# Kernel optimization log

Measured on AMD Instinct MI355X. Metric: run time of the kernel, lower is better.

## Reference

```python
import jax, jax.numpy as jnp
import numpy as np


def setup_inputs() -> dict:
    key = jax.random.key(0)
    ks = jax.random.split(key, 8)
    B, N, D = 8, 2048, 128
    s = 1.0 / float(np.sqrt(D))
    node = jax.random.normal(ks[0], (B, N, D), dtype=jnp.float32)
    node_mask = jax.random.randint(ks[1], (B, N), 0, 2, dtype=jnp.int32)
    punctuation_graph = jax.random.randint(ks[2], (B, N, N), 0, 2, dtype=jnp.int32)
    w_nw = jax.random.uniform(ks[3], (1, D), jnp.float32, -s, s)
    b_nw = jax.random.uniform(ks[4], (1,), jnp.float32, -s, s)
    w_self = jax.random.uniform(ks[5], (D, D), jnp.float32, -s, s)
    b_self = jax.random.uniform(ks[6], (D,), jnp.float32, -s, s)
    w_punct = jax.random.uniform(ks[7], (D, D), jnp.float32, -s, s)
    return {"node": node, "node_mask": node_mask, "punctuation_graph": punctuation_graph,
            "w_nw": w_nw, "b_nw": b_nw, "w_self": w_self, "b_self": b_self,
            "w_punct": w_punct, "iteration_steps": 2}


def reference(node, node_mask, punctuation_graph, w_nw, b_nw, w_self, b_self, w_punct, iteration_steps):
    B, N, D = node.shape
    # dd_graph = mask outer product with zeroed diagonal; graph = dd_graph * punctuation_graph
    eye = jnp.eye(N, dtype=punctuation_graph.dtype)
    dd = node_mask[:, None, :] * node_mask[:, :, None] * (1 - eye)[None, :, :]  # [B,N,N]
    graph = dd * punctuation_graph  # [B,N,N] int, binary
    nbr_num = graph.sum(-1)  # [B,N]
    # replace_masked_values(nbr_num, nbr_num>=1, 1): nodes with no neighbors get denom 1
    nbr_f = jnp.where(nbr_num >= 1, nbr_num.astype(node.dtype), jnp.asarray(1.0, node.dtype))
    gmask = graph > 0
    weights = []
    x = node
    for _ in range(iteration_steps):  # small fixed step count
        dw = jax.nn.sigmoid(jnp.einsum('bnd,od->bno', x, w_nw) + b_nw)[..., 0]  # [B,N]
        weights.append(dw)
        self_info = jnp.einsum('bnd,ed->bne', x, w_self) + b_self  # [B,N,D]
        info_p = jnp.einsum('bnd,ed->bne', x, w_punct)  # [B,N,D]
        # node_weight[b,i,j] = dw[b,j] where graph[b,i,j] else 0
        nw = jnp.where(gmask, dw[:, None, :], jnp.asarray(0.0, x.dtype))  # [B,N,N]
        agg = jnp.einsum('bnm,bmd->bnd', nw, info_p) / nbr_f[..., None]
        x = jax.nn.relu(self_info + agg)
    all_weight = jnp.stack(weights, axis=1)  # [B, steps, N]
    return x, all_weight
```

## Files before the change

### kernel.cpp

```cpp
#include <hip/hip_runtime.h>
#include <hip/hip_bf16.h>

#define BB 8
#define NN 2048
#define DD 128

typedef __attribute__((ext_vector_type(8))) __bf16 bf16x8;
typedef __attribute__((ext_vector_type(4))) float f32x4;
typedef __attribute__((ext_vector_type(4))) int   i32x4;

static __device__ __forceinline__ unsigned short f2bf(float f) {
    union { float f; unsigned u; } v; v.f = f;
    unsigned r = (v.u + 0x7FFFu + ((v.u >> 16) & 1u)) >> 16;
    return (unsigned short)r;
}
static __device__ __forceinline__ float bf2f(unsigned short b) {
    union { unsigned u; float f; } v; v.u = ((unsigned)b) << 16;
    return v.f;
}

__global__ __launch_bounds__(256) void kernP(
    const int* __restrict__ punct, const int* __restrict__ mask,
    unsigned* __restrict__ pk, float* __restrict__ scale_g, float* __restrict__ pdm_g)
{
    const int t = threadIdx.x;
    const int wave = t >> 6, lane = t & 63;
    const int row_g = blockIdx.x * 4 + wave;
    const int b = row_g >> 11;
    const int i = row_g & (NN - 1);

    const int* prow = punct + (size_t)row_g * NN;
    const int* mrow = mask + (size_t)b * NN;

    unsigned pk0 = 0, pk1 = 0;
    int acc = 0;
    #pragma unroll 4
    for (int w = 0; w < 32; ++w) {
        const int col = w * 64 + lane;
        const int p = prow[col];
        const int m = mrow[col];
        const int pred = (p & m) & 1;
        unsigned long long bal = __ballot(pred);
        if (lane == w) { pk0 = (unsigned)bal; pk1 = (unsigned)(bal >> 32); }
        acc += pred + ((col == i ? pred : 0) << 16);
    }
    #pragma unroll
    for (int o = 32; o > 0; o >>= 1) acc += __shfl_xor(acc, o, 64);

    if (lane < 32) {
        uint2 w2; w2.x = pk0; w2.y = pk1;
        *(uint2*)(pk + (size_t)row_g * 64 + 2 * lane) = w2;
    }

    if (lane == 0) {
        const int nall = acc & 0xFFFF;
        const int pdm  = acc >> 16;
        const int mi   = mrow[i];
        const int nbr  = nall - pdm;
        scale_g[row_g] = mi ? 1.f / (float)(nbr < 1 ? 1 : nbr) : 0.f;
        pdm_g[row_g]   = (float)pdm;
    }
}

__global__ __launch_bounds__(256) void kernB(
    const float* __restrict__ x,
    const float* __restrict__ w_nw,  const float* __restrict__ b_nw,
    const float* __restrict__ w_self,const float* __restrict__ b_self,
    const float* __restrict__ w_punct,
    float* __restrict__ si_out,
    unsigned short* __restrict__ yne_out,
    unsigned short* __restrict__ yT_out,
    float* __restrict__ aw_out)
{
    __shared__ unsigned short xt[64*32];
    __shared__ unsigned short wst[128*32];
    __shared__ unsigned short wpt[128*32];
    __shared__ float wnw_l[DD];
    __shared__ float red[256];
    __shared__ float dw_l[64];
    __shared__ unsigned short ytl[128*72];

    const int t  = threadIdx.x;
    const int n0 = blockIdx.x * 64;
    const int b  = n0 >> 11;
    const int nb = n0 & (NN - 1);

    if (t < DD) wnw_l[t] = w_nw[t];
    __syncthreads();

    const int wave = t >> 6, lane = t & 63;
    const int wm = wave >> 1, wn = wave & 1;
    const int quad = lane >> 4, l16 = lane & 15;

    const int n_loc = t >> 2, dq = t & 3;
    const int we = t >> 1,   wh = t & 1;

    f32x4 accs[2][4] = {}; f32x4 accp[2][4] = {};
    float dwpart = 0.f;

    #pragma unroll
    for (int kk = 0; kk < 4; ++kk) {
        const int k0 = kk * 32;
        {
            const float* xs = x + (size_t)(n0 + n_loc) * DD + k0 + dq * 8;
            f32x4 a = *(const f32x4*)xs;
            f32x4 c = *(const f32x4*)(xs + 4);
            const float* wv = &wnw_l[k0 + dq * 8];
            dwpart += a.x*wv[0] + a.y*wv[1] + a.z*wv[2] + a.w*wv[3]
                    + c.x*wv[4] + c.y*wv[5] + c.z*wv[6] + c.w*wv[7];
            unsigned q0 = f2bf(a.x) | ((unsigned)f2bf(a.y) << 16);
            unsigned q1 = f2bf(a.z) | ((unsigned)f2bf(a.w) << 16);
            unsigned q2 = f2bf(c.x) | ((unsigned)f2bf(c.y) << 16);
            unsigned q3 = f2bf(c.z) | ((unsigned)f2bf(c.w) << 16);
            i32x4 pw = {(int)q0,(int)q1,(int)q2,(int)q3};
            *(i32x4*)&xt[n_loc*32 + dq*8] = pw;
        }
        {
            const float* s1 = w_self  + (size_t)we * DD + k0 + wh*16;
            const float* s2 = w_punct + (size_t)we * DD + k0 + wh*16;
            f32x4 a0 = *(const f32x4*)s1;      f32x4 a1 = *(const f32x4*)(s1+4);
            f32x4 a2 = *(const f32x4*)(s1+8);  f32x4 a3 = *(const f32x4*)(s1+12);
            unsigned q0 = f2bf(a0.x) | ((unsigned)f2bf(a0.y)<<16);
            unsigned q1 = f2bf(a0.z) | ((unsigned)f2bf(a0.w)<<16);
            unsigned q2 = f2bf(a1.x) | ((unsigned)f2bf(a1.y)<<16);
            unsigned q3 = f2bf(a1.z) | ((unsigned)f2bf(a1.w)<<16);
            unsigned q4 = f2bf(a2.x) | ((unsigned)f2bf(a2.y)<<16);
            unsigned q5 = f2bf(a2.z) | ((unsigned)f2bf(a2.w)<<16);
            unsigned q6 = f2bf(a3.x) | ((unsigned)f2bf(a3.y)<<16);
            unsigned q7 = f2bf(a3.z) | ((unsigned)f2bf(a3.w)<<16);
            i32x4 pw0 = {(int)q0,(int)q1,(int)q2,(int)q3};
            i32x4 pw1 = {(int)q4,(int)q5,(int)q6,(int)q7};
            *(i32x4*)&wst[we*32 + wh*16]     = pw0;
            *(i32x4*)&wst[we*32 + wh*16 + 8] = pw1;
            f32x4 c0 = *(const f32x4*)s2;      f32x4 c1 = *(const f32x4*)(s2+4);
            f32x4 c2 = *(const f32x4*)(s2+8);  f32x4 c3 = *(const f32x4*)(s2+12);
            unsigned r0 = f2bf(c0.x) | ((unsigned)f2bf(c0.y)<<16);
            unsigned r1 = f2bf(c0.z) | ((unsigned)f2bf(c0.w)<<16);
            unsigned r2 = f2bf(c1.x) | ((unsigned)f2bf(c1.y)<<16);
            unsigned r3 = f2bf(c1.z) | ((unsigned)f2bf(c1.w)<<16);
            unsigned r4 = f2bf(c2.x) | ((unsigned)f2bf(c2.y)<<16);
            unsigned r5 = f2bf(c2.z) | ((unsigned)f2bf(c2.w)<<16);
            unsigned r6 = f2bf(c3.x) | ((unsigned)f2bf(c3.y)<<16);
            unsigned r7 = f2bf(c3.z) | ((unsigned)f2bf(c3.w)<<16);
            i32x4 pv0 = {(int)r0,(int)r1,(int)r2,(int)r3};
            i32x4 pv1 = {(int)r4,(int)r5,(int)r6,(int)r7};
            *(i32x4*)&wpt[we*32 + wh*16]     = pv0;
            *(i32x4*)&wpt[we*32 + wh*16 + 8] = pv1;
        }
        __syncthreads();
        bf16x8 af[2], bs[4], bp[4];
        #pragma unroll
        for (int mt = 0; mt < 2; ++mt)
            af[mt] = *(const bf16x8*)&xt[(wm*32 + mt*16 + l16)*32 + quad*8];
        #pragma unroll
        for (int nt = 0; nt < 4; ++nt) {
            const int er = wn*64 + nt*16 + l16;
            bs[nt] = *(const bf16x8*)&wst[er*32 + quad*8];
            bp[nt] = *(const bf16x8*)&wpt[er*32 + quad*8];
        }
        #pragma unroll
        for (int mt = 0; mt < 2; ++mt)
            #pragma unroll
            for (int nt = 0; nt < 4; ++nt) {
                accs[mt][nt] = __builtin_amdgcn_mfma_f32_16x16x32_bf16(af[mt], bs[nt], accs[mt][nt], 0, 0, 0);
                accp[mt][nt] = __builtin_amdgcn_mfma_f32_16x16x32_bf16(af[mt], bp[nt], accp[mt][nt], 0, 0, 0);
            }
        __syncthreads();
    }

    red[t] = dwpart;
    __syncthreads();
    if (t < 64) {
        float s = red[4*t] + red[4*t+1] + red[4*t+2] + red[4*t+3] + b_nw[0];
        float dv = 1.f / (1.f + __expf(-s));
        dw_l[t] = dv;
        aw_out[(size_t)b * 2 * NN + nb + t] = dv;
    }
    __syncthreads();

    #pragma unroll
    for (int mt = 0; mt < 2; ++mt) {
        #pragma unroll
        for (int nt = 0; nt < 4; ++nt) {
            const int e = wn*64 + nt*16 + l16;
            const float bsv = b_self[e];
            #pragma unroll
            for (int r = 0; r < 4; ++r) {
                const int nl = wm*32 + mt*16 + quad*4 + r;
                const size_t idx = (size_t)(n0 + nl) * DD + e;
                si_out[idx] = accs[mt][nt][r] + bsv;
                const float yv = dw_l[nl] * accp[mt][nt][r];
                const unsigned short ub = f2bf(yv);
                yne_out[idx] = ub;
                ytl[e*72 + nl] = ub;
            }
        }
    }
    __syncthreads();
    {
        const int e = t >> 1, half = t & 1;
        const i32x4* src = (const i32x4*)&ytl[e*72 + half*32];
        i32x4 v0 = src[0], v1 = src[1], v2 = src[2], v3 = src[3];
        i32x4* dst = (i32x4*)(yT_out + (size_t)(b*DD + e) * NN + nb + half*32);
        dst[0] = v0; dst[1] = v1; dst[2] = v2; dst[3] = v3;
    }
}

__global__ __launch_bounds__(256) void kernC(
    const unsigned* __restrict__ pk,
    const float* __restrict__ scale_g, const float* __restrict__ pdm_g,
    const unsigned short* __restrict__ yT,
    const float* __restrict__ si,
    const unsigned short* __restrict__ yne,
    float* __restrict__ x_out)
{
    __shared__ unsigned pPk[64 * 68];
    __shared__ float scale_l[64];
    __shared__ float pdm_l[64];

    const int t  = threadIdx.x;
    const int b  = blockIdx.x >> 5;
    const int i0 = (blockIdx.x & 31) * 64;
    const size_t rg0 = (size_t)b * NN + i0;

    #pragma unroll
    for (int r = 0; r < 4; ++r) {
        const int u   = r * 256 + t;
        const int row = u >> 4;
        const int wq  = (u & 15) * 4;
        i32x4 v = *(const i32x4*)(pk + (rg0 + row) * 64 + wq);
        *(i32x4*)&pPk[row * 68 + wq] = v;
    }
    if (t < 64) {
        scale_l[t] = scale_g[rg0 + t];
        pdm_l[t]   = pdm_g[rg0 + t];
    }
    __syncthreads();

    const int wn = t >> 6, lane = t & 63;
    const int quad = lane >> 4, l16 = lane & 15;
    const unsigned short* yTb = yT + (size_t)b * DD * NN;

    f32x4 acc[4][2] = {};

    #pragma unroll 4
    for (int kk = 0; kk < 64; ++kk) {
        bf16x8 bfr[2];
        #pragma unroll
        for (int nt = 0; nt < 2; ++nt) {
            const int e = wn*32 + nt*16 + l16;
            bfr[nt] = *(const bf16x8*)(yTb + (size_t)e * NN + kk*32 + quad*8);
        }
        bf16x8 af[4];
        #pragma unroll
        for (int mt = 0; mt < 4; ++mt) {
            const unsigned w = pPk[(mt*16 + l16) * 68 + kk];
            const unsigned by = (w >> (quad * 8)) & 0xFFu;
            i32x4 ex;
            ex.x = ((by &   1u) ? 0x3F80 : 0) | ((by &   2u) ? 0x3F800000 : 0);
            ex.y = ((by &   4u) ? 0x3F80 : 0) | ((by &   8u) ? 0x3F800000 : 0);
            ex.z = ((by &  16u) ? 0x3F80 : 0) | ((by &  32u) ? 0x3F800000 : 0);
            ex.w = ((by &  64u) ? 0x3F80 : 0) | ((by & 128u) ? 0x3F800000 : 0);
            union { i32x4 i; bf16x8 h; } cv; cv.i = ex;
            af[mt] = cv.h;
        }
        #pragma unroll
        for (int mt = 0; mt < 4; ++mt)
            #pragma unroll
            for (int nt = 0; nt < 2; ++nt)
                acc[mt][nt] = __builtin_amdgcn_mfma_f32_16x16x32_bf16(af[mt], bfr[nt], acc[mt][nt], 0, 0, 0);
    }

    #pragma unroll
    for (int mt = 0; mt < 4; ++mt) {
        #pragma unroll
        for (int nt = 0; nt < 2; ++nt) {
            const int e = wn*32 + nt*16 + l16;
            #pragma unroll
            for (int r = 0; r < 4; ++r) {
                const int row = mt*16 + quad*4 + r;
                const size_t idx = (rg0 + row) * DD + e;
                const float yv = bf2f(yne[idx]);
                float v = si[idx] + scale_l[row] * (acc[mt][nt][r] - pdm_l[row] * yv);
                x_out[idx] = fmaxf(v, 0.f);
            }
        }
    }
}

extern "C" void kernel_launch(void* const* d_in, const int* in_sizes, int n_in,
                              void* d_out, int out_size, void* d_ws, size_t ws_size,
                              hipStream_t stream) {
    const float* node   = (const float*)d_in[0];
    const int*   mask   = (const int*)  d_in[1];
    const int*   punct  = (const int*)  d_in[2];
    const float* w_nw   = (const float*)d_in[3];
    const float* b_nw   = (const float*)d_in[4];
    const float* w_self = (const float*)d_in[5];
    const float* b_self = (const float*)d_in[6];
    const float* w_punct= (const float*)d_in[7];

    float* xout = (float*)d_out;
    float* aw   = xout + (size_t)BB * NN * DD;

    char* w = (char*)d_ws;
    float*          si   = (float*)w;
    unsigned short* yne  = (unsigned short*)(w + (8u  << 20));
    unsigned short* yT   = (unsigned short*)(w + (12u << 20));
    unsigned*       pk   = (unsigned*)(w + (16u << 20));
    float*          scl  = (float*)(w + (20u << 20));
    float*          pdm  = (float*)(w + (20u << 20) + (64u << 10));

    dim3 blk(256);
    kernP<<<dim3(4096), blk, 0, stream>>>(punct, mask, pk, scl, pdm);
    kernB<<<dim3(256), blk, 0, stream>>>(node, w_nw, b_nw, w_self, b_self, w_punct,
                                         si, yne, yT, aw);
    kernC<<<dim3(256), blk, 0, stream>>>(pk, scl, pdm, yT, si, yne, xout);
    kernB<<<dim3(256), blk, 0, stream>>>(xout, w_nw, b_nw, w_self, b_self, w_punct,
                                         si, yne, yT, aw + NN);
    kernC<<<dim3(256), blk, 0, stream>>>(pk, scl, pdm, yT, si, yne, xout);
}
```

Measured before the change: 286.0 us.

## Pre-convert inputs and weights to bf16, halve tiles, emit bf16 x from aggregation

The bf16 conversion of node, w_self and w_punct moves into the graph-packing kernel as extra blocks. The aggregation kernel now also writes a bf16 copy of x, so the projection kernel reads bf16 operands straight from global memory with no LDS staging or syncs. Both the projection and aggregation kernels switch to 32-row tiles with 512 blocks to raise occupancy on the GPU, and the aggregation kernel's block-to-batch mapping is interleaved. The cost is an extra bf16 write of x per step and more redundant weight reads per block.

```diff
diff --git a/kernel.cpp b/kernel.cpp
--- a/kernel.cpp
+++ b/kernel.cpp
@@ -19,190 +19,167 @@
     return v.f;
 }
 
-__global__ __launch_bounds__(256) void kernP(
+__global__ __launch_bounds__(256) void kernPW(
     const int* __restrict__ punct, const int* __restrict__ mask,
-    unsigned* __restrict__ pk, float* __restrict__ scale_g, float* __restrict__ pdm_g)
+    const float* __restrict__ node, const float* __restrict__ w_self,
+    const float* __restrict__ w_punct,
+    unsigned* __restrict__ pk, float* __restrict__ scale_g, float* __restrict__ pdm_g,
+    unsigned short* __restrict__ xb, unsigned short* __restrict__ wsb,
+    unsigned short* __restrict__ wpb)
 {
     const int t = threadIdx.x;
-    const int wave = t >> 6, lane = t & 63;
-    const int row_g = blockIdx.x * 4 + wave;
-    const int b = row_g >> 11;
-    const int i = row_g & (NN - 1);
-
-    const int* prow = punct + (size_t)row_g * NN;
-    const int* mrow = mask + (size_t)b * NN;
-
-    unsigned pk0 = 0, pk1 = 0;
-    int acc = 0;
-    #pragma unroll 4
-    for (int w = 0; w < 32; ++w) {
-        const int col = w * 64 + lane;
-        const int p = prow[col];
-        const int m = mrow[col];
-        const int pred = (p & m) & 1;
-        unsigned long long bal = __ballot(pred);
-        if (lane == w) { pk0 = (unsigned)bal; pk1 = (unsigned)(bal >> 32); }
-        acc += pred + ((col == i ? pred : 0) << 16);
-    }
-    #pragma unroll
-    for (int o = 32; o > 0; o >>= 1) acc += __shfl_xor(acc, o, 64);
-
-    if (lane < 32) {
-        uint2 w2; w2.x = pk0; w2.y = pk1;
-        *(uint2*)(pk + (size_t)row_g * 64 + 2 * lane) = w2;
-    }
-
-    if (lane == 0) {
-        const int nall = acc & 0xFFFF;
-        const int pdm  = acc >> 16;
-        const int mi   = mrow[i];
-        const int nbr  = nall - pdm;
-        scale_g[row_g] = mi ? 1.f / (float)(nbr < 1 ? 1 : nbr) : 0.f;
-        pdm_g[row_g]   = (float)pdm;
-    }
+    const int bid = blockIdx.x;
+
+    if (bid < 4096) {
+        const int wave = t >> 6, lane = t & 63;
+        const int row_g = bid * 4 + wave;
+        const int b = row_g >> 11;
+        const int i = row_g & (NN - 1);
+
+        const int* prow = punct + (size_t)row_g * NN;
+        const int* mrow = mask + (size_t)b * NN;
+
+        unsigned pk0 = 0, pk1 = 0;
+        int acc = 0;
+        #pragma unroll 4
+        for (int w = 0; w < 32; ++w) {
+            const int col = w * 64 + lane;
+            const int p = prow[col];
+            const int m = mrow[col];
+            const int pred = (p & m) & 1;
+            unsigned long long bal = __ballot(pred);
+            if (lane == w) { pk0 = (unsigned)bal; pk1 = (unsigned)(bal >> 32); }
+            acc += pred + ((col == i ? pred : 0) << 16);
+        }
+        #pragma unroll
+        for (int o = 32; o > 0; o >>= 1) acc += __shfl_xor(acc, o, 64);
+
+        if (lane < 32) {
+            uint2 w2; w2.x = pk0; w2.y = pk1;
+            *(uint2*)(pk + (size_t)row_g * 64 + 2 * lane) = w2;
+        }
+        if (lane == 0) {
+            const int nall = acc & 0xFFFF;
+            const int pdm  = acc >> 16;
+            const int mi   = mrow[i];
+            const int nbr  = nall - pdm;
+            scale_g[row_g] = mi ? 1.f / (float)(nbr < 1 ? 1 : nbr) : 0.f;
+            pdm_g[row_g]   = (float)pdm;
+        }
+        return;
+    }
+
+    const int cb = bid - 4096;
+    const float* src; unsigned short* dst; size_t base;
+    if (cb < 1024)      { src = node;    dst = xb;  base = (size_t)cb * 2048; }
+    else if (cb < 1032) { src = w_self;  dst = wsb; base = (size_t)(cb - 1024) * 2048; }
+    else                { src = w_punct; dst = wpb; base = (size_t)(cb - 1032) * 2048; }
+    const size_t i0 = base + (size_t)t * 8;
+    f32x4 a = *(const f32x4*)(src + i0);
+    f32x4 c = *(const f32x4*)(src + i0 + 4);
+    unsigned q0 = f2bf(a.x) | ((unsigned)f2bf(a.y) << 16);
+    unsigned q1 = f2bf(a.z) | ((unsigned)f2bf(a.w) << 16);
+    unsigned q2 = f2bf(c.x) | ((unsigned)f2bf(c.y) << 16);
+    unsigned q3 = f2bf(c.z) | ((unsigned)f2bf(c.w) << 16);
+    i32x4 pw = {(int)q0, (int)q1, (int)q2, (int)q3};
+    *(i32x4*)(dst + i0) = pw;
 }
 
 __global__ __launch_bounds__(256) void kernB(
-    const float* __restrict__ x,
-    const float* __restrict__ w_nw,  const float* __restrict__ b_nw,
-    const float* __restrict__ w_self,const float* __restrict__ b_self,
-    const float* __restrict__ w_punct,
+    const unsigned short* __restrict__ xb,
+    const float* __restrict__ xf,
+    const unsigned short* __restrict__ wsb,
+    const unsigned short* __restrict__ wpb,
+    const float* __restrict__ w_nw, const float* __restrict__ b_nw,
+    const float* __restrict__ b_self,
     float* __restrict__ si_out,
     unsigned short* __restrict__ yne_out,
     unsigned short* __restrict__ yT_out,
     float* __restrict__ aw_out)
 {
-    __shared__ unsigned short xt[64*32];
-    __shared__ unsigned short wst[128*32];
-    __shared__ unsigned short wpt[128*32];
-    __shared__ float wnw_l[DD];
-    __shared__ float red[256];
-    __shared__ float dw_l[64];
-    __shared__ unsigned short ytl[128*72];
+    __shared__ float dw_l[32];
+    __shared__ unsigned short ytl[128 * 40];
 
     const int t  = threadIdx.x;
-    const int n0 = blockIdx.x * 64;
+    const int n0 = blockIdx.x * 32;
     const int b  = n0 >> 11;
     const int nb = n0 & (NN - 1);
-
-    if (t < DD) wnw_l[t] = w_nw[t];
-    __syncthreads();
-
     const int wave = t >> 6, lane = t & 63;
-    const int wm = wave >> 1, wn = wave & 1;
     const int quad = lane >> 4, l16 = lane & 15;
 
-    const int n_loc = t >> 2, dq = t & 3;
-    const int we = t >> 1,   wh = t & 1;
-
-    f32x4 accs[2][4] = {}; f32x4 accp[2][4] = {};
-    float dwpart = 0.f;
-
+    {
+        const int row = wave * 8 + (lane >> 3);
+        const int seg = (lane & 7) * 16;
+        const float* xr = xf + (size_t)(n0 + row) * DD + seg;
+        const float* wr = w_nw + seg;
+        f32x4 a0 = *(const f32x4*)xr,       a1 = *(const f32x4*)(xr + 4);
+        f32x4 a2 = *(const f32x4*)(xr + 8), a3 = *(const f32x4*)(xr + 12);
+        f32x4 w0 = *(const f32x4*)wr,       w1 = *(const f32x4*)(wr + 4);
+        f32x4 w2 = *(const f32x4*)(wr + 8), w3 = *(const f32x4*)(wr + 12);
+        float s = a0.x*w0.x + a0.y*w0.y + a0.z*w0.z + a0.w*w0.w
+                + a1.x*w1.x + a1.y*w1.y + a1.z*w1.z + a1.w*w1.w
+                + a2.x*w2.x + a2.y*w2.y + a2.z*w2.z + a2.w*w2.w
+                + a3.x*w3.x + a3.y*w3.y + a3.z*w3.z + a3.w*w3.w;
+        s += __shfl_xor(s, 1, 64);
+        s += __shfl_xor(s, 2, 64);
+        s += __shfl_xor(s, 4, 64);
+        if ((lane & 7) == 0) {
+            float dv = 1.f / (1.f + __expf(-(s + b_nw[0])));
+            dw_l[row] = dv;
+            aw_out[(size_t)b * 2 * NN + nb + row] = dv;
+        }
+    }
+
+    f32x4 accs[2][2] = {}, accp[2][2] = {};
+    const unsigned short* xrow = xb + (size_t)n0 * DD;
     #pragma unroll
     for (int kk = 0; kk < 4; ++kk) {
-        const int k0 = kk * 32;
-        {
-            const float* xs = x + (size_t)(n0 + n_loc) * DD + k0 + dq * 8;
-            f32x4 a = *(const f32x4*)xs;
-            f32x4 c = *(const f32x4*)(xs + 4);
-            const float* wv = &wnw_l[k0 + dq * 8];
-            dwpart += a.x*wv[0] + a.y*wv[1] + a.z*wv[2] + a.w*wv[3]
-                    + c.x*wv[4] + c.y*wv[5] + c.z*wv[6] + c.w*wv[7];
-            unsigned q0 = f2bf(a.x) | ((unsigned)f2bf(a.y) << 16);
-            unsigned q1 = f2bf(a.z) | ((unsigned)f2bf(a.w) << 16);
-            unsigned q2 = f2bf(c.x) | ((unsigned)f2bf(c.y) << 16);
-            unsigned q3 = f2bf(c.z) | ((unsigned)f2bf(c.w) << 16);
-            i32x4 pw = {(int)q0,(int)q1,(int)q2,(int)q3};
-            *(i32x4*)&xt[n_loc*32 + dq*8] = pw;
-        }
-        {
-            const float* s1 = w_self  + (size_t)we * DD + k0 + wh*16;
-            const float* s2 = w_punct + (size_t)we * DD + k0 + wh*16;
-            f32x4 a0 = *(const f32x4*)s1;      f32x4 a1 = *(const f32x4*)(s1+4);
-            f32x4 a2 = *(const f32x4*)(s1+8);  f32x4 a3 = *(const f32x4*)(s1+12);
-            unsigned q0 = f2bf(a0.x) | ((unsigned)f2bf(a0.y)<<16);
-            unsigned q1 = f2bf(a0.z) | ((unsigned)f2bf(a0.w)<<16);
-            unsigned q2 = f2bf(a1.x) | ((unsigned)f2bf(a1.y)<<16);
-            unsigned q3 = f2bf(a1.z) | ((unsigned)f2bf(a1.w)<<16);
-            unsigned q4 = f2bf(a2.x) | ((unsigned)f2bf(a2.y)<<16);
-            unsigned q5 = f2bf(a2.z) | ((unsigned)f2bf(a2.w)<<16);
-            unsigned q6 = f2bf(a3.x) | ((unsigned)f2bf(a3.y)<<16);
-            unsigned q7 = f2bf(a3.z) | ((unsigned)f2bf(a3.w)<<16);
-            i32x4 pw0 = {(int)q0,(int)q1,(int)q2,(int)q3};
-            i32x4 pw1 = {(int)q4,(int)q5,(int)q6,(int)q7};
-            *(i32x4*)&wst[we*32 + wh*16]     = pw0;
-            *(i32x4*)&wst[we*32 + wh*16 + 8] = pw1;
-            f32x4 c0 = *(const f32x4*)s2;      f32x4 c1 = *(const f32x4*)(s2+4);
-            f32x4 c2 = *(const f32x4*)(s2+8);  f32x4 c3 = *(const f32x4*)(s2+12);
-            unsigned r0 = f2bf(c0.x) | ((unsigned)f2bf(c0.y)<<16);
-            unsigned r1 = f2bf(c0.z) | ((unsigned)f2bf(c0.w)<<16);
-            unsigned r2 = f2bf(c1.x) | ((unsigned)f2bf(c1.y)<<16);
-            unsigned r3 = f2bf(c1.z) | ((unsigned)f2bf(c1.w)<<16);
-            unsigned r4 = f2bf(c2.x) | ((unsigned)f2bf(c2.y)<<16);
-            unsigned r5 = f2bf(c2.z) | ((unsigned)f2bf(c2.w)<<16);
-            unsigned r6 = f2bf(c3.x) | ((unsigned)f2bf(c3.y)<<16);
-            unsigned r7 = f2bf(c3.z) | ((unsigned)f2bf(c3.w)<<16);
-            i32x4 pv0 = {(int)r0,(int)r1,(int)r2,(int)r3};
-            i32x4 pv1 = {(int)r4,(int)r5,(int)r6,(int)r7};
-            *(i32x4*)&wpt[we*32 + wh*16]     = pv0;
-            *(i32x4*)&wpt[we*32 + wh*16 + 8] = pv1;
-        }
-        __syncthreads();
-        bf16x8 af[2], bs[4], bp[4];
+        const int k0 = kk * 32 + quad * 8;
+        bf16x8 af[2], bs[2], bp[2];
         #pragma unroll
         for (int mt = 0; mt < 2; ++mt)
-            af[mt] = *(const bf16x8*)&xt[(wm*32 + mt*16 + l16)*32 + quad*8];
-        #pragma unroll
-        for (int nt = 0; nt < 4; ++nt) {
-            const int er = wn*64 + nt*16 + l16;
-            bs[nt] = *(const bf16x8*)&wst[er*32 + quad*8];
-            bp[nt] = *(const bf16x8*)&wpt[er*32 + quad*8];
+            af[mt] = *(const bf16x8*)(xrow + (size_t)(mt * 16 + l16) * DD + k0);
+        #pragma unroll
+        for (int nt = 0; nt < 2; ++nt) {
+            const int e = wave * 32 + nt * 16 + l16;
+            bs[nt] = *(const bf16x8*)(wsb + (size_t)e * DD + k0);
+            bp[nt] = *(const bf16x8*)(wpb + (size_t)e * DD + k0);
         }
         #pragma unroll
         for (int mt = 0; mt < 2; ++mt)
             #pragma unroll
-            for (int nt = 0; nt < 4; ++nt) {
+            for (int nt = 0; nt < 2; ++nt) {
                 accs[mt][nt] = __builtin_amdgcn_mfma_f32_16x16x32_bf16(af[mt], bs[nt], accs[mt][nt], 0, 0, 0);
                 accp[mt][nt] = __builtin_amdgcn_mfma_f32_16x16x32_bf16(af[mt], bp[nt], accp[mt][nt], 0, 0, 0);
             }
-        __syncthreads();
-    }
-
-    red[t] = dwpart;
+    }
+
     __syncthreads();
-    if (t < 64) {
-        float s = red[4*t] + red[4*t+1] + red[4*t+2] + red[4*t+3] + b_nw[0];
-        float dv = 1.f / (1.f + __expf(-s));
-        dw_l[t] = dv;
-        aw_out[(size_t)b * 2 * NN + nb + t] = dv;
-    }
-    __syncthreads();
-
     #pragma unroll
     for (int mt = 0; mt < 2; ++mt) {
         #pragma unroll
-        for (int nt = 0; nt < 4; ++nt) {
-            const int e = wn*64 + nt*16 + l16;
+        for (int nt = 0; nt < 2; ++nt) {
+            const int e = wave * 32 + nt * 16 + l16;
             const float bsv = b_self[e];
             #pragma unroll
             for (int r = 0; r < 4; ++r) {
-                const int nl = wm*32 + mt*16 + quad*4 + r;
+                const int nl = mt * 16 + quad * 4 + r;
                 const size_t idx = (size_t)(n0 + nl) * DD + e;
                 si_out[idx] = accs[mt][nt][r] + bsv;
                 const float yv = dw_l[nl] * accp[mt][nt][r];
                 const unsigned short ub = f2bf(yv);
                 yne_out[idx] = ub;
-                ytl[e*72 + nl] = ub;
+                ytl[e * 40 + nl] = ub;
             }
         }
     }
     __syncthreads();
     {
         const int e = t >> 1, half = t & 1;
-        const i32x4* src = (const i32x4*)&ytl[e*72 + half*32];
-        i32x4 v0 = src[0], v1 = src[1], v2 = src[2], v3 = src[3];
-        i32x4* dst = (i32x4*)(yT_out + (size_t)(b*DD + e) * NN + nb + half*32);
-        dst[0] = v0; dst[1] = v1; dst[2] = v2; dst[3] = v3;
+        const i32x4* src = (const i32x4*)&ytl[e * 40 + half * 16];
+        i32x4 v0 = src[0], v1 = src[1];
+        i32x4* dst = (i32x4*)(yT_out + (size_t)(b * DD + e) * NN + nb + half * 16);
+        dst[0] = v0; dst[1] = v1;
     }
 }
 
@@ -212,26 +189,27 @@
     const unsigned short* __restrict__ yT,
     const float* __restrict__ si,
     const unsigned short* __restrict__ yne,
-    float* __restrict__ x_out)
+    float* __restrict__ x_out,
+    unsigned short* __restrict__ xb_out)
 {
-    __shared__ unsigned pPk[64 * 68];
-    __shared__ float scale_l[64];
-    __shared__ float pdm_l[64];
+    __shared__ unsigned pPk[32 * 68];
+    __shared__ float scale_l[32];
+    __shared__ float pdm_l[32];
 
     const int t  = threadIdx.x;
-    const int b  = blockIdx.x >> 5;
-    const int i0 = (blockIdx.x & 31) * 64;
+    const int b  = blockIdx.x & 7;
+    const int i0 = (blockIdx.x >> 3) * 32;
     const size_t rg0 = (size_t)b * NN + i0;
 
     #pragma unroll
-    for (int r = 0; r < 4; ++r) {
+    for (int r = 0; r < 2; ++r) {
         const int u   = r * 256 + t;
         const int row = u >> 4;
         const int wq  = (u & 15) * 4;
         i32x4 v = *(const i32x4*)(pk + (rg0 + row) * 64 + wq);
         *(i32x4*)&pPk[row * 68 + wq] = v;
     }
-    if (t < 64) {
+    if (t < 32) {
         scale_l[t] = scale_g[rg0 + t];
         pdm_l[t]   = pdm_g[rg0 + t];
     }
@@ -241,20 +219,20 @@
     const int quad = lane >> 4, l16 = lane & 15;
     const unsigned short* yTb = yT + (size_t)b * DD * NN;
 
-    f32x4 acc[4][2] = {};
+    f32x4 acc[2][2] = {};
 
     #pragma unroll 4
     for (int kk = 0; kk < 64; ++kk) {
         bf16x8 bfr[2];
         #pragma unroll
         for (int nt = 0; nt < 2; ++nt) {
-            const int e = wn*32 + nt*16 + l16;
-            bfr[nt] = *(const bf16x8*)(yTb + (size_t)e * NN + kk*32 + quad*8);
-        }
-        bf16x8 af[4];
-        #pragma unroll
-        for (int mt = 0; mt < 4; ++mt) {
-            const unsigned w = pPk[(mt*16 + l16) * 68 + kk];
+            const int e = wn * 32 + nt * 16 + l16;
+            bfr[nt] = *(const bf16x8*)(yTb + (size_t)e * NN + kk * 32 + quad * 8);
+        }
+        bf16x8 af[2];
+        #pragma unroll
+        for (int mt = 0; mt < 2; ++mt) {
+            const unsigned w = pPk[(mt * 16 + l16) * 68 + kk];
             const unsigned by = (w >> (quad * 8)) & 0xFFu;
             i32x4 ex;
             ex.x = ((by &   1u) ? 0x3F80 : 0) | ((by &   2u) ? 0x3F800000 : 0);
@@ -265,24 +243,26 @@
             af[mt] = cv.h;
         }
         #pragma unroll
-        for (int mt = 0; mt < 4; ++mt)
+        for (int mt = 0; mt < 2; ++mt)
             #pragma unroll
             for (int nt = 0; nt < 2; ++nt)
                 acc[mt][nt] = __builtin_amdgcn_mfma_f32_16x16x32_bf16(af[mt], bfr[nt], acc[mt][nt], 0, 0, 0);
     }
 
     #pragma unroll
-    for (int mt = 0; mt < 4; ++mt) {
+    for (int mt = 0; mt < 2; ++mt) {
         #pragma unroll
         for (int nt = 0; nt < 2; ++nt) {
-            const int e = wn*32 + nt*16 + l16;
+            const int e = wn * 32 + nt * 16 + l16;
             #pragma unroll
             for (int r = 0; r < 4; ++r) {
-                const int row = mt*16 + quad*4 + r;
+                const int row = mt * 16 + quad * 4 + r;
                 const size_t idx = (rg0 + row) * DD + e;
                 const float yv = bf2f(yne[idx]);
                 float v = si[idx] + scale_l[row] * (acc[mt][nt][r] - pdm_l[row] * yv);
-                x_out[idx] = fmaxf(v, 0.f);
+                v = fmaxf(v, 0.f);
+                x_out[idx]  = v;
+                xb_out[idx] = f2bf(v);
             }
         }
     }
@@ -310,13 +290,17 @@
     unsigned*       pk   = (unsigned*)(w + (16u << 20));
     float*          scl  = (float*)(w + (20u << 20));
     float*          pdm  = (float*)(w + (20u << 20) + (64u << 10));
+    unsigned short* xb   = (unsigned short*)(w + (21u << 20));
+    unsigned short* wsb  = (unsigned short*)(w + (25u << 20));
+    unsigned short* wpb  = (unsigned short*)(w + (25u << 20) + (32u << 10));
 
     dim3 blk(256);
-    kernP<<<dim3(4096), blk, 0, stream>>>(punct, mask, pk, scl, pdm);
-    kernB<<<dim3(256), blk, 0, stream>>>(node, w_nw, b_nw, w_self, b_self, w_punct,
+    kernPW<<<dim3(5136), blk, 0, stream>>>(punct, mask, node, w_self, w_punct,
+                                           pk, scl, pdm, xb, wsb, wpb);
+    kernB<<<dim3(512), blk, 0, stream>>>(xb, node, wsb, wpb, w_nw, b_nw, b_self,
                                          si, yne, yT, aw);
-    kernC<<<dim3(256), blk, 0, stream>>>(pk, scl, pdm, yT, si, yne, xout);
-    kernB<<<dim3(256), blk, 0, stream>>>(xout, w_nw, b_nw, w_self, b_self, w_punct,
+    kernC<<<dim3(512), blk, 0, stream>>>(pk, scl, pdm, yT, si, yne, xout, xb);
+    kernB<<<dim3(512), blk, 0, stream>>>(xb, xout, wsb, wpb, w_nw, b_nw, b_self,
                                          si, yne, yT, aw + NN);
-    kernC<<<dim3(256), blk, 0, stream>>>(pk, scl, pdm, yT, si, yne, xout);
-}
+    kernC<<<dim3(512), blk, 0, stream>>>(pk, scl, pdm, yT, si, yne, xout, xb);
+}
```

Result: slower. 304.3 us (+6.4%).

## Fuse graph packing with first projection kernel and cache bf16 weights

Applied to the files above, without the earlier changes.

Merges the punctuation-graph bit-packing kernel, the first-step projection kernel and a weight bf16 conversion into a single launch using block-index dispatch, so the small projection work overlaps with the bandwidth-bound packing pass. The second-step projection reads pre-converted bf16 weights instead of reconverting fp32. kernC's block-to-batch mapping is also permuted so neighbouring blocks cover different batches. The cost is a larger, heterogeneous kernel whose shared-memory footprint applies to the packing blocks too, which may reduce their occupancy.

```diff
diff --git a/kernel.cpp b/kernel.cpp
--- a/kernel.cpp
+++ b/kernel.cpp
@@ -19,54 +19,12 @@
     return v.f;
 }
 
-__global__ __launch_bounds__(256) void kernP(
-    const int* __restrict__ punct, const int* __restrict__ mask,
-    unsigned* __restrict__ pk, float* __restrict__ scale_g, float* __restrict__ pdm_g)
-{
-    const int t = threadIdx.x;
-    const int wave = t >> 6, lane = t & 63;
-    const int row_g = blockIdx.x * 4 + wave;
-    const int b = row_g >> 11;
-    const int i = row_g & (NN - 1);
-
-    const int* prow = punct + (size_t)row_g * NN;
-    const int* mrow = mask + (size_t)b * NN;
-
-    unsigned pk0 = 0, pk1 = 0;
-    int acc = 0;
-    #pragma unroll 4
-    for (int w = 0; w < 32; ++w) {
-        const int col = w * 64 + lane;
-        const int p = prow[col];
-        const int m = mrow[col];
-        const int pred = (p & m) & 1;
-        unsigned long long bal = __ballot(pred);
-        if (lane == w) { pk0 = (unsigned)bal; pk1 = (unsigned)(bal >> 32); }
-        acc += pred + ((col == i ? pred : 0) << 16);
-    }
-    #pragma unroll
-    for (int o = 32; o > 0; o >>= 1) acc += __shfl_xor(acc, o, 64);
-
-    if (lane < 32) {
-        uint2 w2; w2.x = pk0; w2.y = pk1;
-        *(uint2*)(pk + (size_t)row_g * 64 + 2 * lane) = w2;
-    }
-
-    if (lane == 0) {
-        const int nall = acc & 0xFFFF;
-        const int pdm  = acc >> 16;
-        const int mi   = mrow[i];
-        const int nbr  = nall - pdm;
-        scale_g[row_g] = mi ? 1.f / (float)(nbr < 1 ? 1 : nbr) : 0.f;
-        pdm_g[row_g]   = (float)pdm;
-    }
-}
-
-__global__ __launch_bounds__(256) void kernB(
-    const float* __restrict__ x,
+template <bool PRECONV>
+static __device__ __forceinline__ void kernB_body(
+    int n0, const float* __restrict__ x,
     const float* __restrict__ w_nw,  const float* __restrict__ b_nw,
-    const float* __restrict__ w_self,const float* __restrict__ b_self,
-    const float* __restrict__ w_punct,
+    const void* __restrict__ wself_p, const float* __restrict__ b_self,
+    const void* __restrict__ wpunct_p,
     float* __restrict__ si_out,
     unsigned short* __restrict__ yne_out,
     unsigned short* __restrict__ yT_out,
@@ -81,7 +39,6 @@
     __shared__ unsigned short ytl[128*72];
 
     const int t  = threadIdx.x;
-    const int n0 = blockIdx.x * 64;
     const int b  = n0 >> 11;
     const int nb = n0 & (NN - 1);
 
@@ -115,9 +72,20 @@
             i32x4 pw = {(int)q0,(int)q1,(int)q2,(int)q3};
             *(i32x4*)&xt[n_loc*32 + dq*8] = pw;
         }
-        {
-            const float* s1 = w_self  + (size_t)we * DD + k0 + wh*16;
-            const float* s2 = w_punct + (size_t)we * DD + k0 + wh*16;
+        if (PRECONV) {
+            const unsigned short* s1 = (const unsigned short*)wself_p  + (size_t)we * DD + k0 + wh*16;
+            const unsigned short* s2 = (const unsigned short*)wpunct_p + (size_t)we * DD + k0 + wh*16;
+            i32x4 a0 = *(const i32x4*)s1;
+            i32x4 a1 = *(const i32x4*)(s1 + 8);
+            *(i32x4*)&wst[we*32 + wh*16]     = a0;
+            *(i32x4*)&wst[we*32 + wh*16 + 8] = a1;
+            i32x4 c0 = *(const i32x4*)s2;
+            i32x4 c1 = *(const i32x4*)(s2 + 8);
+            *(i32x4*)&wpt[we*32 + wh*16]     = c0;
+            *(i32x4*)&wpt[we*32 + wh*16 + 8] = c1;
+        } else {
+            const float* s1 = (const float*)wself_p  + (size_t)we * DD + k0 + wh*16;
+            const float* s2 = (const float*)wpunct_p + (size_t)we * DD + k0 + wh*16;
             f32x4 a0 = *(const f32x4*)s1;      f32x4 a1 = *(const f32x4*)(s1+4);
             f32x4 a2 = *(const f32x4*)(s1+8);  f32x4 a3 = *(const f32x4*)(s1+12);
             unsigned q0 = f2bf(a0.x) | ((unsigned)f2bf(a0.y)<<16);
@@ -206,6 +174,90 @@
     }
 }
 
+__global__ __launch_bounds__(256) void kern0(
+    const int* __restrict__ punct, const int* __restrict__ mask,
+    const float* __restrict__ node,
+    const float* __restrict__ w_nw, const float* __restrict__ b_nw,
+    const float* __restrict__ w_self, const float* __restrict__ b_self,
+    const float* __restrict__ w_punct,
+    unsigned* __restrict__ pk, float* __restrict__ scale_g, float* __restrict__ pdm_g,
+    unsigned short* __restrict__ wsb, unsigned short* __restrict__ wpb,
+    float* __restrict__ si, unsigned short* __restrict__ yne,
+    unsigned short* __restrict__ yT, float* __restrict__ aw)
+{
+    const int bid = blockIdx.x;
+    const int t = threadIdx.x;
+
+    if (bid < 256) {
+        kernB_body<false>(bid * 64, node, w_nw, b_nw, w_self, b_self, w_punct,
+                          si, yne, yT, aw);
+        return;
+    }
+    if (bid < 272) {
+        const int cb = bid - 256;
+        const float* src = (cb < 8) ? w_self : w_punct;
+        unsigned short* dst = (cb < 8) ? wsb : wpb;
+        const size_t i0 = (size_t)(cb & 7) * 2048 + (size_t)t * 8;
+        f32x4 a = *(const f32x4*)(src + i0);
+        f32x4 c = *(const f32x4*)(src + i0 + 4);
+        unsigned q0 = f2bf(a.x) | ((unsigned)f2bf(a.y) << 16);
+        unsigned q1 = f2bf(a.z) | ((unsigned)f2bf(a.w) << 16);
+        unsigned q2 = f2bf(c.x) | ((unsigned)f2bf(c.y) << 16);
+        unsigned q3 = f2bf(c.z) | ((unsigned)f2bf(c.w) << 16);
+        i32x4 pw = {(int)q0, (int)q1, (int)q2, (int)q3};
+        *(i32x4*)(dst + i0) = pw;
+        return;
+    }
+
+    const int wave = t >> 6, lane = t & 63;
+    const int row_g = (bid - 272) * 4 + wave;
+    const int b = row_g >> 11;
+    const int i = row_g & (NN - 1);
+
+    const int* prow = punct + (size_t)row_g * NN;
+    const int* mrow = mask + (size_t)b * NN;
+
+    unsigned pk0 = 0, pk1 = 0;
+    int acc = 0;
+    #pragma unroll 4
+    for (int w = 0; w < 32; ++w) {
+        const int col = w * 64 + lane;
+        const int p = prow[col];
+        const int m = mrow[col];
+        const int pred = (p & m) & 1;
+        unsigned long long bal = __ballot(pred);
+        if (lane == w) { pk0 = (unsigned)bal; pk1 = (unsigned)(bal >> 32); }
+        acc += pred + ((col == i ? pred : 0) << 16);
+    }
+    #pragma unroll
+    for (int o = 32; o > 0; o >>= 1) acc += __shfl_xor(acc, o, 64);
+
+    if (lane < 32) {
+        uint2 w2; w2.x = pk0; w2.y = pk1;
+        *(uint2*)(pk + (size_t)row_g * 64 + 2 * lane) = w2;
+    }
+    if (lane == 0) {
+        const int nall = acc & 0xFFFF;
+        const int pdm  = acc >> 16;
+        const int mi   = mrow[i];
+        const int nbr  = nall - pdm;
+        scale_g[row_g] = mi ? 1.f / (float)(nbr < 1 ? 1 : nbr) : 0.f;
+        pdm_g[row_g]   = (float)pdm;
+    }
+}
+
+__global__ __launch_bounds__(256) void kernB1(
+    const float* __restrict__ x,
+    const unsigned short* __restrict__ wsb, const unsigned short* __restrict__ wpb,
+    const float* __restrict__ w_nw, const float* __restrict__ b_nw,
+    const float* __restrict__ b_self,
+    float* __restrict__ si, unsigned short* __restrict__ yne,
+    unsigned short* __restrict__ yT, float* __restrict__ aw1)
+{
+    kernB_body<true>(blockIdx.x * 64, x, w_nw, b_nw, wsb, b_self, wpb,
+                     si, yne, yT, aw1);
+}
+
 __global__ __launch_bounds__(256) void kernC(
     const unsigned* __restrict__ pk,
     const float* __restrict__ scale_g, const float* __restrict__ pdm_g,
@@ -219,8 +271,8 @@
     __shared__ float pdm_l[64];
 
     const int t  = threadIdx.x;
-    const int b  = blockIdx.x >> 5;
-    const int i0 = (blockIdx.x & 31) * 64;
+    const int b  = blockIdx.x & 7;
+    const int i0 = (blockIdx.x >> 3) * 64;
     const size_t rg0 = (size_t)b * NN + i0;
 
     #pragma unroll
@@ -310,13 +362,16 @@
     unsigned*       pk   = (unsigned*)(w + (16u << 20));
     float*          scl  = (float*)(w + (20u << 20));
     float*          pdm  = (float*)(w + (20u << 20) + (64u << 10));
+    unsigned short* wsb  = (unsigned short*)(w + (21u << 20));
+    unsigned short* wpb  = (unsigned short*)(w + (21u << 20) + (32u << 10));
 
     dim3 blk(256);
-    kernP<<<dim3(4096), blk, 0, stream>>>(punct, mask, pk, scl, pdm);
-    kernB<<<dim3(256), blk, 0, stream>>>(node, w_nw, b_nw, w_self, b_self, w_punct,
-                                         si, yne, yT, aw);
+    kern0<<<dim3(4368), blk, 0, stream>>>(punct, mask, node, w_nw, b_nw,
+                                          w_self, b_self, w_punct,
+                                          pk, scl, pdm, wsb, wpb,
+                                          si, yne, yT, aw);
     kernC<<<dim3(256), blk, 0, stream>>>(pk, scl, pdm, yT, si, yne, xout);
-    kernB<<<dim3(256), blk, 0, stream>>>(xout, w_nw, b_nw, w_self, b_self, w_punct,
-                                         si, yne, yT, aw + NN);
+    kernB1<<<dim3(256), blk, 0, stream>>>(xout, wsb, wpb, w_nw, b_nw, b_self,
+                                          si, yne, yT, aw + NN);
     kernC<<<dim3(256), blk, 0, stream>>>(pk, scl, pdm, yT, si, yne, xout);
 }
```

Result: slower. 299.7 us (+4.8%).
